# Performance work log

Hardware: AMD Instinct MI355X
Metric: run time of the kernel (lower is better)

The kernel has to match this reference:

```python
import jax, jax.numpy as jnp
import numpy as np

B, N_IN, D_IN = 2048, 49, 320
D = 768            # inner_dim
H = 8              # n_heads
DH = D // H        # head dim = 96
NQ = 8             # n_queries
D_OUT = 3072       # llama_hidden
EPS = 1e-5


def _ln(x, g, b):
    mu = jnp.mean(x, axis=-1, keepdims=True)
    var = jnp.mean(jnp.square(x - mu), axis=-1, keepdims=True)
    return (x - mu) * jax.lax.rsqrt(var + EPS) * g + b


def setup_inputs() -> dict:
    key = jax.random.key(0)
    ks = jax.random.split(key, 16)
    s = lambda k, shape, fan: jax.random.normal(k, shape, jnp.float32) * (1.0 / np.sqrt(fan))
    return {
        "features": jax.random.normal(ks[0], (B, N_IN, D_IN), jnp.float32),
        "input_proj_w": s(ks[1], (D, D_IN), D_IN),
        "input_proj_b": jnp.zeros((D,), jnp.float32),
        "queries": jax.random.normal(ks[2], (NQ, D), jnp.float32) * 0.02,
        "ln_q_g": jnp.ones((D,), jnp.float32), "ln_q_b": jnp.zeros((D,), jnp.float32),
        "ln_kv_g": jnp.ones((D,), jnp.float32), "ln_kv_b": jnp.zeros((D,), jnp.float32),
        "in_proj_w": s(ks[3], (3 * D, D), D),
        "in_proj_b": jnp.zeros((3 * D,), jnp.float32),
        "out_proj_w": s(ks[4], (D, D), D),
        "out_proj_b": jnp.zeros((D,), jnp.float32),
        "ln_ff_g": jnp.ones((D,), jnp.float32), "ln_ff_b": jnp.zeros((D,), jnp.float32),
        "ffn_w1": s(ks[5], (D, D), D), "ffn_b1": jnp.zeros((D,), jnp.float32),
        "ffn_w2": s(ks[6], (D, D), D), "ffn_b2": jnp.zeros((D,), jnp.float32),
        "output_proj_w": s(ks[7], (D_OUT, D), D),
        "output_proj_b": jnp.zeros((D_OUT,), jnp.float32),
        "final_g": jnp.ones((D_OUT,), jnp.float32), "final_b": jnp.zeros((D_OUT,), jnp.float32),
    }


def reference(features, input_proj_w, input_proj_b, queries,
              ln_q_g, ln_q_b, ln_kv_g, ln_kv_b,
              in_proj_w, in_proj_b, out_proj_w, out_proj_b,
              ln_ff_g, ln_ff_b, ffn_w1, ffn_b1, ffn_w2, ffn_b2,
              output_proj_w, output_proj_b, final_g, final_b):
    b = features.shape[0]
    # kv projection: (B, N_in, D)
    kv = jnp.einsum('bnd,ed->bne', features, input_proj_w) + input_proj_b
    q = jnp.broadcast_to(queries[None], (b, NQ, D))

    # --- single layer (n_layers=1) ---
    q_norm = _ln(q, ln_q_g, ln_q_b)
    kv_norm = _ln(kv, ln_kv_g, ln_kv_b)

    wq, wk, wv = in_proj_w[:D], in_proj_w[D:2 * D], in_proj_w[2 * D:]
    bq, bk, bv = in_proj_b[:D], in_proj_b[D:2 * D], in_proj_b[2 * D:]
    qp = (jnp.einsum('bqd,ed->bqe', q_norm, wq) + bq).reshape(b, NQ, H, DH)
    kp = (jnp.einsum('bnd,ed->bne', kv_norm, wk) + bk).reshape(b, N_IN, H, DH)
    vp = (jnp.einsum('bnd,ed->bne', kv_norm, wv) + bv).reshape(b, N_IN, H, DH)

    scores = jnp.einsum('bqhd,bnhd->bhqn', qp, kp) / np.sqrt(DH).astype(np.float32)
    attn = jax.nn.softmax(scores, axis=-1)
    ctx = jnp.einsum('bhqn,bnhd->bqhd', attn, vp).reshape(b, NQ, D)
    attn_out = jnp.einsum('bqd,ed->bqe', ctx, out_proj_w) + out_proj_b

    q = q + attn_out
    h = _ln(q, ln_ff_g, ln_ff_b)
    h = jnp.einsum('bqd,ed->bqe', h, ffn_w1) + ffn_b1
    h = jax.nn.gelu(h, approximate=False)
    h = jnp.einsum('bqd,ed->bqe', h, ffn_w2) + ffn_b2
    q = q + h

    out = jnp.einsum('bqd,ed->bqe', q, output_proj_w) + output_proj_b
    return _ln(out, final_g, final_b)
```

## Files before the change

### kernel.cpp

```cpp
#include <hip/hip_runtime.h>
#include <math.h>

typedef __attribute__((ext_vector_type(8))) short short8;
typedef __attribute__((ext_vector_type(8))) unsigned short ushort8;
typedef __attribute__((ext_vector_type(4))) float f32x4;

__device__ __forceinline__ float b2f(unsigned short h) {
    union { unsigned int u; float f; } c; c.u = ((unsigned int)h) << 16; return c.f;
}
__device__ __forceinline__ unsigned short f2b(float x) {
    union { float f; unsigned int u; } c; c.f = x;
    unsigned int r = c.u + 0x7fffu + ((c.u >> 16) & 1u);
    return (unsigned short)(r >> 16);
}

__global__ __launch_bounds__(256) void cast_f2b(const float* __restrict__ in,
                                                unsigned short* __restrict__ out, int n4) {
    int i = blockIdx.x * 256 + threadIdx.x;
    if (i >= n4) return;
    float4 f = ((const float4*)in)[i];
    ushort4 o; o.x = f2b(f.x); o.y = f2b(f.y); o.z = f2b(f.z); o.w = f2b(f.w);
    ((ushort4*)out)[i] = o;
}

template <int DD, bool INB, bool OUTB>
__global__ __launch_bounds__(256) void ln_rows(const void* __restrict__ in_, void* __restrict__ out_,
                                               const float* __restrict__ g, const float* __restrict__ bb,
                                               int nrows) {
    const int wv = threadIdx.x >> 6, l = threadIdx.x & 63;
    const int row = blockIdx.x * 4 + wv;
    if (row >= nrows) return;
    constexpr int NC = DD / 256;
    float v[DD / 64];
    if constexpr (INB) {
        const ushort4* in = (const ushort4*)((const unsigned short*)in_ + (size_t)row * DD);
#pragma unroll
        for (int c = 0; c < NC; ++c) {
            ushort4 u = in[l + 64 * c];
            v[4*c] = b2f(u.x); v[4*c+1] = b2f(u.y); v[4*c+2] = b2f(u.z); v[4*c+3] = b2f(u.w);
        }
    } else {
        const float4* in = (const float4*)((const float*)in_ + (size_t)row * DD);
#pragma unroll
        for (int c = 0; c < NC; ++c) {
            float4 u = in[l + 64 * c];
            v[4*c] = u.x; v[4*c+1] = u.y; v[4*c+2] = u.z; v[4*c+3] = u.w;
        }
    }
    float s = 0.f, s2 = 0.f;
#pragma unroll
    for (int i = 0; i < DD / 64; ++i) { s += v[i]; s2 += v[i] * v[i]; }
#pragma unroll
    for (int o = 32; o > 0; o >>= 1) { s += __shfl_xor(s, o, 64); s2 += __shfl_xor(s2, o, 64); }
    const float mu = s * (1.0f / DD);
    const float var = s2 * (1.0f / DD) - mu * mu;
    const float rs = rsqrtf(var + 1e-5f);
    if constexpr (OUTB) {
        ushort4* out = (ushort4*)((unsigned short*)out_ + (size_t)row * DD);
#pragma unroll
        for (int c = 0; c < NC; ++c) {
            int e = (l + 64 * c) * 4;
            ushort4 o4;
            o4.x = f2b((v[4*c]   - mu) * rs * g[e]   + bb[e]);
            o4.y = f2b((v[4*c+1] - mu) * rs * g[e+1] + bb[e+1]);
            o4.z = f2b((v[4*c+2] - mu) * rs * g[e+2] + bb[e+2]);
            o4.w = f2b((v[4*c+3] - mu) * rs * g[e+3] + bb[e+3]);
            out[l + 64 * c] = o4;
        }
    } else {
        float4* out = (float4*)((float*)out_ + (size_t)row * DD);
#pragma unroll
        for (int c = 0; c < NC; ++c) {
            int e = (l + 64 * c) * 4;
            float4 o4;
            o4.x = (v[4*c]   - mu) * rs * g[e]   + bb[e];
            o4.y = (v[4*c+1] - mu) * rs * g[e+1] + bb[e+1];
            o4.z = (v[4*c+2] - mu) * rs * g[e+2] + bb[e+2];
            o4.w = (v[4*c+3] - mu) * rs * g[e+3] + bb[e+3];
            out[l + 64 * c] = o4;
        }
    }
}

__global__ __launch_bounds__(256) void ln_stats(const unsigned short* __restrict__ kv,
                                                float2* __restrict__ stats, int nrows) {
    const int wv = threadIdx.x >> 6, l = threadIdx.x & 63;
    const int row = blockIdx.x * 4 + wv;
    if (row >= nrows) return;
    const ushort4* in = (const ushort4*)(kv + (size_t)row * 768);
    float s = 0.f, s2 = 0.f;
#pragma unroll
    for (int c = 0; c < 3; ++c) {
        ushort4 u = in[l + 64 * c];
        float a = b2f(u.x), b = b2f(u.y), cc = b2f(u.z), d = b2f(u.w);
        s += a + b + cc + d;
        s2 += a * a + b * b + cc * cc + d * d;
    }
#pragma unroll
    for (int o = 32; o > 0; o >>= 1) { s += __shfl_xor(s, o, 64); s2 += __shfl_xor(s2, o, 64); }
    const float mu = s * (1.0f / 768.0f);
    const float var = s2 * (1.0f / 768.0f) - mu * mu;
    const float rs = rsqrtf(var + 1e-5f);
    if (l == 0) stats[row] = make_float2(rs, rs * mu);
}

__global__ __launch_bounds__(256) void qp_kernel(const float* __restrict__ qn, const float* __restrict__ wq,
                                                 const float* __restrict__ bq, float* __restrict__ qp) {
    int q = blockIdx.x / 3;
    int col = (blockIdx.x % 3) * 256 + threadIdx.x;
    const float4* a = (const float4*)(qn + q * 768);
    const float4* wr = (const float4*)(wq + (size_t)col * 768);
    float s = 0.f;
#pragma unroll 8
    for (int k = 0; k < 192; ++k) {
        float4 xx = a[k], yy = wr[k];
        s += xx.x * yy.x + xx.y * yy.y + xx.z * yy.z + xx.w * yy.w;
    }
    qp[q * 768 + col] = s + bq[col];
}

__global__ __launch_bounds__(256) void qk_build(const float* __restrict__ qp, const float* __restrict__ wk,
                                                const float* __restrict__ g,
                                                unsigned short* __restrict__ qkg, float* __restrict__ tout) {
    __shared__ float red[4];
    const int hq = blockIdx.x, h = hq >> 3, q = hq & 7;
    const int tid = threadIdx.x;
    const float* qv = qp + q * 768 + h * 96;
    float tsum = 0.f;
#pragma unroll
    for (int c = 0; c < 3; ++c) {
        int e = tid + 256 * c;
        float s = 0.f;
        for (int d = 0; d < 96; ++d) s += qv[d] * wk[(size_t)(h * 96 + d) * 768 + e];
        unsigned short bv = f2b(s * 0.10206207262f * g[e]);
        qkg[hq * 768 + e] = bv;
        tsum += b2f(bv);
    }
#pragma unroll
    for (int o = 32; o > 0; o >>= 1) tsum += __shfl_xor(tsum, o, 64);
    if ((tid & 63) == 0) red[tid >> 6] = tsum;
    __syncthreads();
    if (tid == 0) tout[hq] = red[0] + red[1] + red[2] + red[3];
}

__device__ __forceinline__ void gll16(const void* g, void* l) {
    __builtin_amdgcn_global_load_lds((const __attribute__((address_space(1))) unsigned int*)g,
                                     (__attribute__((address_space(3))) unsigned int*)l, 16, 0, 0);
}

template <int ROWS>
__device__ __forceinline__ void stage_rows(const unsigned short* gbase, int ldg,
                                           unsigned short* lds, int tid) {
    int wuni = tid & ~63;
#pragma unroll
    for (int it = 0; it < ROWS / 32; ++it) {
        int s = it * 256 + tid;
        int r = s >> 3, c = s & 7;
        int cc = c ^ (r & 7);
        gll16(gbase + (size_t)r * ldg + cc * 8, lds + (size_t)(it * 256 + wuni) * 8);
    }
}

template <int EPI>
__global__ __launch_bounds__(256) void gemm_bf16(
    const unsigned short* __restrict__ A, const unsigned short* __restrict__ W,
    const float* __restrict__ bias, void* __restrict__ out,
    const float* __restrict__ aux, int K, int N) {
    __shared__ __align__(16) unsigned short lA[128 * 64];
    __shared__ __align__(16) unsigned short lB[128 * 64];
    const int tid = threadIdx.x;
    const int l = tid & 63, w = tid >> 6;
    int gx = gridDim.x;
    int lid = blockIdx.y * gx + blockIdx.x;
    int nwg = gx * gridDim.y;
    int idx = (nwg & 7) ? lid : ((lid & 7) * (nwg >> 3) + (lid >> 3));
    const int bm0 = (idx / gx) * 128, bn0 = (idx % gx) * 128;
    const int wm = (w >> 1) * 64, wn = (w & 1) * 64;
    const int l15 = l & 15, lk = l >> 4;
    f32x4 acc[4][4] = {};
    const int nk = K >> 6;
    const unsigned short* Abase = A + (size_t)bm0 * K;
    const unsigned short* Wbase = W + (size_t)bn0 * K;
    for (int kt = 0; kt < nk; ++kt) {
        stage_rows<128>(Abase + kt * 64, K, lA, tid);
        stage_rows<128>(Wbase + kt * 64, K, lB, tid);
        __syncthreads();
        short8 af[4], bf[4];
#pragma unroll
        for (int kk = 0; kk < 2; ++kk) {
#pragma unroll
            for (int mf = 0; mf < 4; ++mf) {
                int r = wm + mf * 16 + l15;
                int c = (kk * 4 + lk) ^ (r & 7);
                af[mf] = *(const short8*)(lA + r * 64 + c * 8);
            }
#pragma unroll
            for (int nf = 0; nf < 4; ++nf) {
                int r = wn + nf * 16 + l15;
                int c = (kk * 4 + lk) ^ (r & 7);
                bf[nf] = *(const short8*)(lB + r * 64 + c * 8);
            }
#pragma unroll
            for (int mf = 0; mf < 4; ++mf)
#pragma unroll
                for (int nf = 0; nf < 4; ++nf)
                    acc[mf][nf] = __builtin_amdgcn_mfma_f32_16x16x32_bf16(af[mf], bf[nf], acc[mf][nf], 0, 0, 0);
        }
        __syncthreads();
    }
    const int row0 = bm0 + wm + (lk << 2);
    const int col0 = bn0 + wn + l15;
#pragma unroll
    for (int nf = 0; nf < 4; ++nf) {
        int col = col0 + nf * 16;
        float bv = bias[col];
#pragma unroll
        for (int mf = 0; mf < 4; ++mf) {
#pragma unroll
            for (int r = 0; r < 4; ++r) {
                int row = row0 + mf * 16 + r;
                float v = acc[mf][nf][r] + bv;
                size_t idx2 = (size_t)row * N + col;
                if constexpr (EPI == 0) {
                    ((unsigned short*)out)[idx2] = f2b(v);
                } else if constexpr (EPI == 1) {
                    v += aux[(row & 7) * N + col];
                    ((float*)out)[idx2] = v;
                } else if constexpr (EPI == 2) {
                    v = 0.5f * v * (1.0f + erff(v * 0.70710678118f));
                    ((unsigned short*)out)[idx2] = f2b(v);
                } else if constexpr (EPI == 3) {
                    v += aux[idx2];
                    ((unsigned short*)out)[idx2] = f2b(v);
                } else {
                    ((float*)out)[idx2] = v;
                }
            }
        }
    }
}

__global__ __launch_bounds__(256) void gemm_scores(const unsigned short* __restrict__ A,
                                                   const unsigned short* __restrict__ Qk,
                                                   const float2* __restrict__ stats,
                                                   const float* __restrict__ tcol,
                                                   float* __restrict__ S) {
    __shared__ __align__(16) unsigned short lA[128 * 64];
    __shared__ __align__(16) unsigned short lB[64 * 64];
    const int tid = threadIdx.x;
    const int l = tid & 63, w = tid >> 6;
    int lid = blockIdx.x;
    int idx = (lid & 7) * (gridDim.x >> 3) + (lid >> 3);
    const int bm0 = idx * 128;
    const int wm = (w >> 1) * 64, wn = (w & 1) * 32;
    const int l15 = l & 15, lk = l >> 4;
    f32x4 acc[4][2] = {};
    const unsigned short* Abase = A + (size_t)bm0 * 768;
    for (int kt = 0; kt < 12; ++kt) {
        stage_rows<128>(Abase + kt * 64, 768, lA, tid);
        stage_rows<64>(Qk + kt * 64, 768, lB, tid);
        __syncthreads();
        short8 af[4], bf[2];
#pragma unroll
        for (int kk = 0; kk < 2; ++kk) {
#pragma unroll
            for (int mf = 0; mf < 4; ++mf) {
                int r = wm + mf * 16 + l15;
                int c = (kk * 4 + lk) ^ (r & 7);
                af[mf] = *(const short8*)(lA + r * 64 + c * 8);
            }
#pragma unroll
            for (int nf = 0; nf < 2; ++nf) {
                int r = wn + nf * 16 + l15;
                int c = (kk * 4 + lk) ^ (r & 7);
                bf[nf] = *(const short8*)(lB + r * 64 + c * 8);
            }
#pragma unroll
            for (int mf = 0; mf < 4; ++mf)
#pragma unroll
                for (int nf = 0; nf < 2; ++nf)
                    acc[mf][nf] = __builtin_amdgcn_mfma_f32_16x16x32_bf16(af[mf], bf[nf], acc[mf][nf], 0, 0, 0);
        }
        __syncthreads();
    }
    const int row0 = bm0 + wm + (lk << 2);
    const int col0 = wn + l15;
    const float tv0 = tcol[col0], tv1 = tcol[col0 + 16];
#pragma unroll
    for (int mf = 0; mf < 4; ++mf)
#pragma unroll
        for (int r = 0; r < 4; ++r) {
            int row = row0 + mf * 16 + r;
            float2 st = stats[row];
            S[(size_t)row * 64 + col0]      = st.x * acc[mf][0][r] - st.y * tv0;
            S[(size_t)row * 64 + col0 + 16] = st.x * acc[mf][1][r] - st.y * tv1;
        }
}

__global__ __launch_bounds__(256) void attn_mix(const unsigned short* __restrict__ kvr,
                                                const float* __restrict__ S,
                                                const float2* __restrict__ stats,
                                                const float* __restrict__ lg,
                                                const float* __restrict__ lb,
                                                unsigned short* __restrict__ cmix) {
    __shared__ __align__(16) unsigned short at[64 * 64];
    __shared__ __align__(16) unsigned short kvT[192 * 64];
    __shared__ float dl[64];
    float* Sl = (float*)kvT;
    const int b = blockIdx.x;
    const int t = threadIdx.x, l = t & 63, w = t >> 6;
    const int l15 = l & 15, lk = l >> 4;

    for (int i = t; i < 3136; i += 256) Sl[i] = S[(size_t)b * 3136 + i];
    __syncthreads();
    if (w == 0) {
        float mx = -1e30f;
        for (int n = 0; n < 49; ++n) mx = fmaxf(mx, Sl[n * 64 + l]);
        float sum = 0.f;
        for (int n = 0; n < 49; ++n) sum += __expf(Sl[n * 64 + l] - mx);
        float inv = 1.0f / sum;
        float dacc = 0.f;
#pragma unroll
        for (int c = 0; c < 8; ++c) {
            int cc = c ^ (l & 7);
            for (int j = 0; j < 8; ++j) {
                int n = c * 8 + j;
                float av = 0.f;
                if (n < 49) {
                    float a = __expf(Sl[n * 64 + l] - mx) * inv;
                    float2 st = stats[(size_t)b * 49 + n];
                    av = a * st.x;
                    dacc += a * st.y;
                }
                at[l * 64 + cc * 8 + j] = f2b(av);
            }
        }
        dl[l] = dacc;
    }
    __syncthreads();

    float dlv[4][4];
#pragma unroll
    for (int mf = 0; mf < 4; ++mf)
#pragma unroll
        for (int r = 0; r < 4; ++r) dlv[mf][r] = dl[mf * 16 + lk * 4 + r];

    const unsigned short* src = kvr + ((size_t)b * 49 + (l < 49 ? l : 0)) * 768;
#pragma unroll 1
    for (int ph = 0; ph < 4; ++ph) {
#pragma unroll
        for (int i = 0; i < 6; ++i) {
            int e0 = w * 8 + i * 32;
            ushort8 v = {0, 0, 0, 0, 0, 0, 0, 0};
            if (l < 49) v = *(const ushort8*)(src + ph * 192 + e0);
#pragma unroll
            for (int j = 0; j < 8; ++j) {
                int e = e0 + j;
                kvT[e * 64 + (((l >> 3) ^ (e & 7)) << 3) + (l & 7)] = v[j];
            }
        }
        __syncthreads();
        f32x4 acc[4][3] = {};
#pragma unroll
        for (int ks = 0; ks < 2; ++ks) {
            short8 af[4], bf[3];
#pragma unroll
            for (int mf = 0; mf < 4; ++mf) {
                int r = mf * 16 + l15;
                af[mf] = *(const short8*)(at + r * 64 + (((ks * 4 + lk) ^ (r & 7)) << 3));
            }
#pragma unroll
            for (int nf = 0; nf < 3; ++nf) {
                int er = w * 48 + nf * 16 + l15;
                bf[nf] = *(const short8*)(kvT + er * 64 + (((ks * 4 + lk) ^ (er & 7)) << 3));
            }
#pragma unroll
            for (int mf = 0; mf < 4; ++mf)
#pragma unroll
                for (int nf = 0; nf < 3; ++nf)
                    acc[mf][nf] = __builtin_amdgcn_mfma_f32_16x16x32_bf16(af[mf], bf[nf], acc[mf][nf], 0, 0, 0);
        }
#pragma unroll
        for (int nf = 0; nf < 3; ++nf) {
            int e = ph * 192 + w * 48 + nf * 16 + l15;
            float gg = lg[e], bbv = lb[e];
#pragma unroll
            for (int mf = 0; mf < 4; ++mf)
#pragma unroll
                for (int r = 0; r < 4; ++r) {
                    int hq = mf * 16 + lk * 4 + r;
                    float val = gg * (acc[mf][nf][r] - dlv[mf][r]) + bbv;
                    cmix[((size_t)(hq >> 3) * 16384 + b * 8 + (hq & 7)) * 768 + e] = f2b(val);
                }
        }
        __syncthreads();
    }
}

__global__ __launch_bounds__(256) void gemm_ctx(const unsigned short* __restrict__ cmix,
                                                const unsigned short* __restrict__ wvb,
                                                const float* __restrict__ bv,
                                                unsigned short* __restrict__ ctx) {
    __shared__ __align__(16) unsigned short lA[128 * 64];
    __shared__ __align__(16) unsigned short lB[128 * 64];
    const int tid = threadIdx.x;
    const int l = tid & 63, w = tid >> 6;
    const int h = blockIdx.z;
    int yy = blockIdx.y;
    int idx = (yy & 7) * 16 + (yy >> 3);
    const int bm0 = idx * 128;
    const int wm = (w >> 1) * 64, wn = (w & 1) * 64;
    const int l15 = l & 15, lk = l >> 4;
    f32x4 acc[4][4] = {};
    const unsigned short* Abase = cmix + (size_t)h * 16384 * 768 + (size_t)bm0 * 768;
    const unsigned short* Wbase = wvb + (size_t)h * 96 * 768;
    for (int kt = 0; kt < 12; ++kt) {
        stage_rows<128>(Abase + kt * 64, 768, lA, tid);
        stage_rows<128>(Wbase + kt * 64, 768, lB, tid);
        __syncthreads();
        short8 af[4], bf[4];
#pragma unroll
        for (int kk = 0; kk < 2; ++kk) {
#pragma unroll
            for (int mf = 0; mf < 4; ++mf) {
                int r = wm + mf * 16 + l15;
                int c = (kk * 4 + lk) ^ (r & 7);
                af[mf] = *(const short8*)(lA + r * 64 + c * 8);
            }
#pragma unroll
            for (int nf = 0; nf < 4; ++nf) {
                int r = wn + nf * 16 + l15;
                int c = (kk * 4 + lk) ^ (r & 7);
                bf[nf] = *(const short8*)(lB + r * 64 + c * 8);
            }
#pragma unroll
            for (int mf = 0; mf < 4; ++mf)
#pragma unroll
                for (int nf = 0; nf < 4; ++nf)
                    acc[mf][nf] = __builtin_amdgcn_mfma_f32_16x16x32_bf16(af[mf], bf[nf], acc[mf][nf], 0, 0, 0);
        }
        __syncthreads();
    }
    const int row0 = bm0 + wm + (lk << 2);
    const int col0 = wn + l15;
#pragma unroll
    for (int nf = 0; nf < 4; ++nf) {
        int col = col0 + nf * 16;
        if (col >= 96) continue;
        float bvv = bv[h * 96 + col];
#pragma unroll
        for (int mf = 0; mf < 4; ++mf)
#pragma unroll
            for (int r = 0; r < 4; ++r) {
                int row = row0 + mf * 16 + r;
                ctx[(size_t)row * 768 + h * 96 + col] = f2b(acc[mf][nf][r] + bvv);
            }
    }
}

extern "C" void kernel_launch(void* const* d_in, const int* in_sizes, int n_in,
                              void* d_out, int out_size, void* d_ws, size_t ws_size,
                              hipStream_t stream) {
    (void)in_sizes; (void)n_in; (void)out_size;
    const float* features      = (const float*)d_in[0];
    const float* input_proj_w  = (const float*)d_in[1];
    const float* input_proj_b  = (const float*)d_in[2];
    const float* queries       = (const float*)d_in[3];
    const float* ln_q_g        = (const float*)d_in[4];
    const float* ln_q_b        = (const float*)d_in[5];
    const float* ln_kv_g       = (const float*)d_in[6];
    const float* ln_kv_b       = (const float*)d_in[7];
    const float* in_proj_w     = (const float*)d_in[8];
    const float* in_proj_b     = (const float*)d_in[9];
    const float* out_proj_w    = (const float*)d_in[10];
    const float* out_proj_b    = (const float*)d_in[11];
    const float* ln_ff_g       = (const float*)d_in[12];
    const float* ln_ff_b       = (const float*)d_in[13];
    const float* ffn_w1        = (const float*)d_in[14];
    const float* ffn_b1        = (const float*)d_in[15];
    const float* ffn_w2        = (const float*)d_in[16];
    const float* ffn_b2        = (const float*)d_in[17];
    const float* output_proj_w = (const float*)d_in[18];
    const float* output_proj_b = (const float*)d_in[19];
    const float* final_g       = (const float*)d_in[20];
    const float* final_b       = (const float*)d_in[21];

    char* ws = (char*)d_ws;
    size_t off = 0;
    auto alloc = [&](size_t bytes) -> char* {
        char* r = ws + off; off += (bytes + 255) & ~(size_t)255; return r;
    };
    unsigned short* featb = (unsigned short*)alloc(100352ull * 320 * 2);
    unsigned short* kvbuf = (unsigned short*)alloc(100352ull * 768 * 2);
    unsigned short* cmix  = (unsigned short*)alloc(8ull * 16384 * 768 * 2);
    float*          S     = (float*)alloc(100352ull * 64 * 4);
    float2*         stats = (float2*)alloc(100352ull * 8);
    unsigned short* winb  = (unsigned short*)alloc(768ull * 320 * 2);
    unsigned short* wvb   = (unsigned short*)alloc(768ull * 768 * 2);
    unsigned short* woutb = (unsigned short*)alloc(768ull * 768 * 2);
    unsigned short* w1b   = (unsigned short*)alloc(768ull * 768 * 2);
    unsigned short* w2b   = (unsigned short*)alloc(768ull * 768 * 2);
    unsigned short* wopb  = (unsigned short*)alloc(3072ull * 768 * 2);
    float* qnorm          = (float*)alloc(8 * 768 * 4);
    float* qpb            = (float*)alloc(8 * 768 * 4);
    unsigned short* qkb   = (unsigned short*)alloc(64ull * 768 * 2);
    float* tbuf           = (float*)alloc(64 * 4);
    if (off > ws_size) return;

    unsigned short* ctx  = featb;
    unsigned short* outb = kvbuf;
    float* x             = (float*)cmix;
    unsigned short* hn   = (unsigned short*)((char*)cmix + 50331648);
    unsigned short* f1   = (unsigned short*)((char*)cmix + 75497472);
    unsigned short* x2   = (unsigned short*)((char*)cmix + 100663296);

    cast_f2b<<<31360, 256, 0, stream>>>(features, featb, 8028160);
    cast_f2b<<<240,   256, 0, stream>>>(input_proj_w, winb, 61440);
    cast_f2b<<<576,   256, 0, stream>>>(in_proj_w + 2 * 768 * 768, wvb, 147456);
    cast_f2b<<<576,   256, 0, stream>>>(out_proj_w, woutb, 147456);
    cast_f2b<<<576,   256, 0, stream>>>(ffn_w1, w1b, 147456);
    cast_f2b<<<576,   256, 0, stream>>>(ffn_w2, w2b, 147456);
    cast_f2b<<<2304,  256, 0, stream>>>(output_proj_w, wopb, 589824);

    ln_rows<768, false, false><<<2, 256, 0, stream>>>(queries, qnorm, ln_q_g, ln_q_b, 8);
    qp_kernel<<<24, 256, 0, stream>>>(qnorm, in_proj_w, in_proj_b, qpb);
    qk_build<<<64, 256, 0, stream>>>(qpb, in_proj_w + 768 * 768, ln_kv_g, qkb, tbuf);

    gemm_bf16<0><<<dim3(6, 784), 256, 0, stream>>>(featb, winb, input_proj_b, kvbuf, nullptr, 320, 768);
    ln_stats<<<25088, 256, 0, stream>>>(kvbuf, stats, 100352);
    gemm_scores<<<784, 256, 0, stream>>>(kvbuf, qkb, stats, tbuf, S);
    attn_mix<<<2048, 256, 0, stream>>>(kvbuf, S, stats, ln_kv_g, ln_kv_b, cmix);
    gemm_ctx<<<dim3(1, 128, 8), 256, 0, stream>>>(cmix, wvb, in_proj_b + 1536, ctx);
    gemm_bf16<1><<<dim3(6, 128), 256, 0, stream>>>(ctx, woutb, out_proj_b, x, queries, 768, 768);
    ln_rows<768, false, true><<<4096, 256, 0, stream>>>(x, hn, ln_ff_g, ln_ff_b, 16384);
    gemm_bf16<2><<<dim3(6, 128), 256, 0, stream>>>(hn, w1b, ffn_b1, f1, nullptr, 768, 768);
    gemm_bf16<3><<<dim3(6, 128), 256, 0, stream>>>(f1, w2b, ffn_b2, x2, x, 768, 768);
    gemm_bf16<0><<<dim3(24, 128), 256, 0, stream>>>(x2, wopb, output_proj_b, outb, nullptr, 768, 3072);
    ln_rows<3072, true, false><<<4096, 256, 0, stream>>>(outb, (float*)d_out, final_g, final_b, 16384);
}
```

Before: 756.8 us.

## Merge weight casts into one launch and restructure attn_mix with prefetch

The seven fp32-to-bf16 cast launches become a single kernel that picks its source tensor from the block index, removing launch overhead and the gaps between launches. attn_mix now spreads the softmax and attention-weight construction across all four waves instead of only wave 0. It also processes 128-column phases with the global kv loads for the next phase prefetched into registers, and swaps the MFMA operands so each lane writes four contiguous bf16 outputs per store instead of scalar ones. This reduces LDS footprint and serialized work, at the cost of more register pressure and redundant exp computation in every wave.

```diff
diff --git a/kernel.cpp b/kernel.cpp
--- a/kernel.cpp
+++ b/kernel.cpp
@@ -14,13 +14,26 @@
     return (unsigned short)(r >> 16);
 }
 
-__global__ __launch_bounds__(256) void cast_f2b(const float* __restrict__ in,
-                                                unsigned short* __restrict__ out, int n4) {
-    int i = blockIdx.x * 256 + threadIdx.x;
-    if (i >= n4) return;
-    float4 f = ((const float4*)in)[i];
-    ushort4 o; o.x = f2b(f.x); o.y = f2b(f.y); o.z = f2b(f.z); o.w = f2b(f.w);
-    ((ushort4*)out)[i] = o;
+__global__ __launch_bounds__(256) void cast_all(
+    const float* __restrict__ f,    unsigned short* __restrict__ fb,
+    const float* __restrict__ winw, unsigned short* __restrict__ winb,
+    const float* __restrict__ wv,   unsigned short* __restrict__ wvb,
+    const float* __restrict__ wo,   unsigned short* __restrict__ wob,
+    const float* __restrict__ w1,   unsigned short* __restrict__ w1b,
+    const float* __restrict__ w2,   unsigned short* __restrict__ w2b,
+    const float* __restrict__ wop,  unsigned short* __restrict__ wopb) {
+    int blk = blockIdx.x;
+    const float* src; unsigned short* dst; int i;
+    if (blk < 31360)      { src = f;    dst = fb;   i = blk * 256 + threadIdx.x; }
+    else if (blk < 31600) { src = winw; dst = winb; i = (blk - 31360) * 256 + threadIdx.x; }
+    else if (blk < 32176) { src = wv;   dst = wvb;  i = (blk - 31600) * 256 + threadIdx.x; }
+    else if (blk < 32752) { src = wo;   dst = wob;  i = (blk - 32176) * 256 + threadIdx.x; }
+    else if (blk < 33328) { src = w1;   dst = w1b;  i = (blk - 32752) * 256 + threadIdx.x; }
+    else if (blk < 33904) { src = w2;   dst = w2b;  i = (blk - 33328) * 256 + threadIdx.x; }
+    else                  { src = wop;  dst = wopb; i = (blk - 33904) * 256 + threadIdx.x; }
+    float4 fv = ((const float4*)src)[i];
+    ushort4 o; o.x = f2b(fv.x); o.y = f2b(fv.y); o.z = f2b(fv.z); o.w = f2b(fv.w);
+    ((ushort4*)dst)[i] = o;
 }
 
 template <int DD, bool INB, bool OUTB>
@@ -304,7 +317,7 @@
                                                 const float* __restrict__ lb,
                                                 unsigned short* __restrict__ cmix) {
     __shared__ __align__(16) unsigned short at[64 * 64];
-    __shared__ __align__(16) unsigned short kvT[192 * 64];
+    __shared__ __align__(16) unsigned short kvT[128 * 64];
     __shared__ float dl[64];
     float* Sl = (float*)kvT;
     const int b = blockIdx.x;
@@ -312,87 +325,105 @@
     const int l15 = l & 15, lk = l >> 4;
 
     for (int i = t; i < 3136; i += 256) Sl[i] = S[(size_t)b * 3136 + i];
+
+    const unsigned short* src = kvr + ((size_t)b * 49 + (l < 49 ? l : 0)) * 768;
+    ushort8 z8 = {0, 0, 0, 0, 0, 0, 0, 0};
+    ushort8 va0 = z8, va1 = z8, va2 = z8, va3 = z8;
+    if (l < 49) {
+        va0 = *(const ushort8*)(src + w * 8);
+        va1 = *(const ushort8*)(src + w * 8 + 32);
+        va2 = *(const ushort8*)(src + w * 8 + 64);
+        va3 = *(const ushort8*)(src + w * 8 + 96);
+    }
     __syncthreads();
-    if (w == 0) {
-        float mx = -1e30f;
-        for (int n = 0; n < 49; ++n) mx = fmaxf(mx, Sl[n * 64 + l]);
-        float sum = 0.f;
-        for (int n = 0; n < 49; ++n) sum += __expf(Sl[n * 64 + l] - mx);
-        float inv = 1.0f / sum;
-        float dacc = 0.f;
-#pragma unroll
-        for (int c = 0; c < 8; ++c) {
-            int cc = c ^ (l & 7);
-            for (int j = 0; j < 8; ++j) {
-                int n = c * 8 + j;
-                float av = 0.f;
-                if (n < 49) {
-                    float a = __expf(Sl[n * 64 + l] - mx) * inv;
-                    float2 st = stats[(size_t)b * 49 + n];
-                    av = a * st.x;
-                    dacc += a * st.y;
-                }
-                at[l * 64 + cc * 8 + j] = f2b(av);
-            }
-        }
-        dl[l] = dacc;
-    }
+
+    float mx = -1e30f;
+    for (int n = 0; n < 49; ++n) mx = fmaxf(mx, Sl[n * 64 + l]);
+    float sum = 0.f, dun = 0.f;
+    for (int n = 0; n < 49; ++n) {
+        float e = __expf(Sl[n * 64 + l] - mx);
+        sum += e;
+        dun += e * stats[(size_t)b * 49 + n].y;
+    }
+    float inv = 1.0f / sum;
+#pragma unroll
+    for (int cd = 0; cd < 2; ++cd) {
+        int c = w * 2 + cd;
+        int cc = c ^ (l & 7);
+#pragma unroll
+        for (int j = 0; j < 8; ++j) {
+            int n = c * 8 + j;
+            float av = 0.f;
+            if (n < 49) av = __expf(Sl[n * 64 + l] - mx) * inv * stats[(size_t)b * 49 + n].x;
+            at[l * 64 + cc * 8 + j] = f2b(av);
+        }
+    }
+    if (w == 0) dl[l] = dun * inv;
     __syncthreads();
 
-    float dlv[4][4];
-#pragma unroll
-    for (int mf = 0; mf < 4; ++mf)
-#pragma unroll
-        for (int r = 0; r < 4; ++r) dlv[mf][r] = dl[mf * 16 + lk * 4 + r];
-
-    const unsigned short* src = kvr + ((size_t)b * 49 + (l < 49 ? l : 0)) * 768;
+    float dls[4];
+#pragma unroll
+    for (int nf = 0; nf < 4; ++nf) dls[nf] = dl[nf * 16 + l15];
+
 #pragma unroll 1
-    for (int ph = 0; ph < 4; ++ph) {
-#pragma unroll
-        for (int i = 0; i < 6; ++i) {
+    for (int ph = 0; ph < 6; ++ph) {
+#pragma unroll
+        for (int i = 0; i < 4; ++i) {
+            ushort8 v = (i == 0) ? va0 : (i == 1) ? va1 : (i == 2) ? va2 : va3;
             int e0 = w * 8 + i * 32;
-            ushort8 v = {0, 0, 0, 0, 0, 0, 0, 0};
-            if (l < 49) v = *(const ushort8*)(src + ph * 192 + e0);
 #pragma unroll
             for (int j = 0; j < 8; ++j) {
                 int e = e0 + j;
                 kvT[e * 64 + (((l >> 3) ^ (e & 7)) << 3) + (l & 7)] = v[j];
             }
         }
-        __syncthreads();
-        f32x4 acc[4][3] = {};
+        ushort8 nb0 = z8, nb1 = z8, nb2 = z8, nb3 = z8;
+        if (ph < 5 && l < 49) {
+            const unsigned short* s2 = src + (ph + 1) * 128 + w * 8;
+            nb0 = *(const ushort8*)(s2);
+            nb1 = *(const ushort8*)(s2 + 32);
+            nb2 = *(const ushort8*)(s2 + 64);
+            nb3 = *(const ushort8*)(s2 + 96);
+        }
+        __syncthreads();
+        f32x4 acc[2][4] = {};
 #pragma unroll
         for (int ks = 0; ks < 2; ++ks) {
-            short8 af[4], bf[3];
-#pragma unroll
-            for (int mf = 0; mf < 4; ++mf) {
-                int r = mf * 16 + l15;
-                af[mf] = *(const short8*)(at + r * 64 + (((ks * 4 + lk) ^ (r & 7)) << 3));
-            }
-#pragma unroll
-            for (int nf = 0; nf < 3; ++nf) {
-                int er = w * 48 + nf * 16 + l15;
-                bf[nf] = *(const short8*)(kvT + er * 64 + (((ks * 4 + lk) ^ (er & 7)) << 3));
-            }
-#pragma unroll
-            for (int mf = 0; mf < 4; ++mf)
-#pragma unroll
-                for (int nf = 0; nf < 3; ++nf)
+            short8 af[2], bf[4];
+#pragma unroll
+            for (int mf = 0; mf < 2; ++mf) {
+                int r = w * 32 + mf * 16 + l15;
+                af[mf] = *(const short8*)(kvT + r * 64 + (((ks * 4 + lk) ^ (r & 7)) << 3));
+            }
+#pragma unroll
+            for (int nf = 0; nf < 4; ++nf) {
+                int r = nf * 16 + l15;
+                bf[nf] = *(const short8*)(at + r * 64 + (((ks * 4 + lk) ^ (r & 7)) << 3));
+            }
+#pragma unroll
+            for (int mf = 0; mf < 2; ++mf)
+#pragma unroll
+                for (int nf = 0; nf < 4; ++nf)
                     acc[mf][nf] = __builtin_amdgcn_mfma_f32_16x16x32_bf16(af[mf], bf[nf], acc[mf][nf], 0, 0, 0);
         }
 #pragma unroll
-        for (int nf = 0; nf < 3; ++nf) {
-            int e = ph * 192 + w * 48 + nf * 16 + l15;
-            float gg = lg[e], bbv = lb[e];
-#pragma unroll
-            for (int mf = 0; mf < 4; ++mf)
-#pragma unroll
-                for (int r = 0; r < 4; ++r) {
-                    int hq = mf * 16 + lk * 4 + r;
-                    float val = gg * (acc[mf][nf][r] - dlv[mf][r]) + bbv;
-                    cmix[((size_t)(hq >> 3) * 16384 + b * 8 + (hq & 7)) * 768 + e] = f2b(val);
-                }
-        }
+        for (int mf = 0; mf < 2; ++mf) {
+            int e0 = ph * 128 + w * 32 + mf * 16 + lk * 4;
+            float4 g4 = *(const float4*)(lg + e0);
+            float4 b4 = *(const float4*)(lb + e0);
+#pragma unroll
+            for (int nf = 0; nf < 4; ++nf) {
+                int hq = nf * 16 + l15;
+                float dv = dls[nf];
+                ushort4 o;
+                o.x = f2b(g4.x * (acc[mf][nf][0] - dv) + b4.x);
+                o.y = f2b(g4.y * (acc[mf][nf][1] - dv) + b4.y);
+                o.z = f2b(g4.z * (acc[mf][nf][2] - dv) + b4.z);
+                o.w = f2b(g4.w * (acc[mf][nf][3] - dv) + b4.w);
+                *(ushort4*)(cmix + ((size_t)(hq >> 3) * 16384 + b * 8 + (hq & 7)) * 768 + e0) = o;
+            }
+        }
+        va0 = nb0; va1 = nb1; va2 = nb2; va3 = nb3;
         __syncthreads();
     }
 }
@@ -514,13 +545,9 @@
     unsigned short* f1   = (unsigned short*)((char*)cmix + 75497472);
     unsigned short* x2   = (unsigned short*)((char*)cmix + 100663296);
 
-    cast_f2b<<<31360, 256, 0, stream>>>(features, featb, 8028160);
-    cast_f2b<<<240,   256, 0, stream>>>(input_proj_w, winb, 61440);
-    cast_f2b<<<576,   256, 0, stream>>>(in_proj_w + 2 * 768 * 768, wvb, 147456);
-    cast_f2b<<<576,   256, 0, stream>>>(out_proj_w, woutb, 147456);
-    cast_f2b<<<576,   256, 0, stream>>>(ffn_w1, w1b, 147456);
-    cast_f2b<<<576,   256, 0, stream>>>(ffn_w2, w2b, 147456);
-    cast_f2b<<<2304,  256, 0, stream>>>(output_proj_w, wopb, 589824);
+    cast_all<<<36208, 256, 0, stream>>>(features, featb, input_proj_w, winb,
+                                        in_proj_w + 2 * 768 * 768, wvb, out_proj_w, woutb,
+                                        ffn_w1, w1b, ffn_w2, w2b, output_proj_w, wopb);
 
     ln_rows<768, false, false><<<2, 256, 0, stream>>>(queries, qnorm, ln_q_g, ln_q_b, 8);
     qp_kernel<<<24, 256, 0, stream>>>(qnorm, in_proj_w, in_proj_b, qpb);
```

Result: faster. 734.9 us (-2.9%).
